# Kernel optimization log

Measured on AMD Instinct MI355X. Metric: run time of the kernel, lower is better.

The kernel has to match this reference:

```python
import jax, jax.numpy as jnp
import numpy as np
from jax import lax

NUM_CHANNELS = 32
PROT_SECTION = 4
PROT_SIZE = NUM_CHANNELS * PROT_SECTION  # 128
BATCH = 128
SEQ_LEN = 8194


def setup_inputs() -> dict:
    key = jax.random.key(0)
    ks = jax.random.split(key, 6)
    input_seq = jax.random.randint(ks[0], (BATCH, SEQ_LEN), 0, 26)
    emb = jax.random.normal(ks[1], (26, 5), dtype=jnp.float32)
    conv_w = jax.random.normal(ks[2], (NUM_CHANNELS, 5, 3), dtype=jnp.float32) * 0.1
    conv_b = jnp.zeros((NUM_CHANNELS,), dtype=jnp.float32)
    W_a = jax.random.normal(ks[3], (PROT_SIZE, PROT_SIZE), dtype=jnp.float32) / np.sqrt(PROT_SIZE)
    v_a = jax.random.normal(ks[4], (PROT_SIZE,), dtype=jnp.float32)
    return {"input_seq": input_seq, "emb": emb, "conv_w": conv_w,
            "conv_b": conv_b, "W_a": W_a, "v_a": v_a}


def reference(input_seq, emb, conv_w, conv_b, W_a, v_a):
    # Embedding lookup: [B, L, 5] -> [B, 5, L]
    x = emb[input_seq].transpose(0, 2, 1)
    # Conv1d(5 -> C, k=3, valid) + bias + ReLU  (dropout is identity in eval)
    y = lax.conv_general_dilated(x, conv_w, window_strides=(1,), padding='VALID',
                                 dimension_numbers=('NCH', 'OIH', 'NCH'))
    y = jax.nn.relu(y + conv_b[None, :, None])  # [B, C, L-2]
    B, C, PL = y.shape
    S = PROT_SECTION
    new_L = PL // S
    rem = PL % S
    head = rem // 2
    tail = PL - (rem - head)
    y = y[:, :, head:tail].reshape(B, C * S, new_L)  # [B, D, N], D = C*S
    # Batched self-attention pooling (original loops over batch in Python)
    # energies[b, n] = v_a @ tanh(W_a @ H_b)
    e = jnp.einsum('d,bdn->bn', v_a, jnp.tanh(jnp.einsum('de,ben->bdn', W_a, y)))
    w = jax.nn.softmax(e, axis=-1)  # stable softmax; same math as unstable F.softmax
    ctx = jnp.einsum('bn,bdn->bd', w, y)  # [B, D]
    return ctx
```

## Files before the change

### kernel.cpp

```cpp
#include <hip/hip_runtime.h>

#define LSEQ 8194
#define NPOS 2048

typedef _Float16 f16x8 __attribute__((ext_vector_type(8)));
typedef _Float16 f16x2 __attribute__((ext_vector_type(2)));
typedef __attribute__((ext_vector_type(4))) float f32x4;

static __device__ __forceinline__ float tanh_fast(float x){
    float p = __expf(2.0f * x);
    float r = __builtin_amdgcn_rcpf(1.0f + p);
    return 1.0f - 2.0f * r;
}
static __device__ __forceinline__ unsigned h3relu(unsigned a, unsigned b, unsigned c){
    union { f16x2 h; unsigned u; } x, y, z, r;
    x.u = a; y.u = b; z.u = c;
    f16x2 s = x.h + y.h + z.h;
    f16x2 zero = { (_Float16)0.0f, (_Float16)0.0f };
    r.h = __builtin_elementwise_max(s, zero);
    return r.u;
}
static __device__ __forceinline__ unsigned hpack(float a, float b){
    union { f16x2 h; unsigned u; } pk;
    pk.h = (f16x2){ (_Float16)a, (_Float16)b };
    return pk.u;
}

__global__ __launch_bounds__(256) void k_tbl(
        const float* __restrict__ emb, const float* __restrict__ cw,
        const float* __restrict__ cb, const float* __restrict__ Wa,
        unsigned* __restrict__ tblp, unsigned* __restrict__ wah)
{
    int gid = blockIdx.x*256 + threadIdx.x;
    if (gid < 1248){
        int k = gid / 416;
        int rem = gid - k*416;
        int l = rem >> 4;
        int cp = rem & 15;
        int c0 = cp*2;
        float v0 = 0.f, v1 = 0.f;
        #pragma unroll
        for (int i = 0; i < 5; i++){
            float e = emb[l*5 + i];
            v0 += cw[(c0*5 + i)*3 + k] * e;
            v1 += cw[((c0+1)*5 + i)*3 + k] * e;
        }
        if (k == 2){ v0 += cb[c0]; v1 += cb[c0+1]; }
        tblp[k*520 + l*20 + (cp & 3)*4 + (cp >> 2)] = hpack(v0, v1);
    }
    for (int i = gid; i < 8192; i += 1280)
        wah[i] = hpack(Wa[2*i], Wa[2*i + 1]);
}

__global__ __launch_bounds__(256, 4) void ka_conv_gemm(
        const int* __restrict__ seq, const unsigned* __restrict__ tblp,
        const unsigned* __restrict__ wah, const float* __restrict__ va,
        float* __restrict__ ws_e)
{
    __shared__ __align__(16) unsigned tblH[1560];
    __shared__ unsigned short seqw16[4][132];
    __shared__ uint4 bshare[16*64];
    __shared__ float epar[4][64];

    int tid = threadIdx.x;
    int b   = blockIdx.y;
    int n0  = blockIdx.x * 128;

    for (int i = tid; i < 390; i += 256)
        ((uint4*)tblH)[i] = ((const uint4*)tblp)[i];
    const int* sb = seq + (size_t)b * LSEQ;
    for (int i = tid; i < 4*130; i += 256){
        int s = i / 130, off = i - s*130;
        seqw16[s][off] = (unsigned short)(sb[s*2048 + n0 + off] * 80);
    }

    int w = tid >> 6, lane = tid & 63;
    int m = lane & 15, q = lane >> 4;

    uint4 wfu[2][4];
    #pragma unroll
    for (int dtL = 0; dtL < 2; dtL++)
        #pragma unroll
        for (int ki = 0; ki < 4; ki++)
            wfu[dtL][ki] = *(const uint4*)((const char*)wah +
                ((2*w+dtL)*16 + m)*256 + ki*64 + q*16);
    float varg[2][4];
    #pragma unroll
    for (int dtL = 0; dtL < 2; dtL++)
        #pragma unroll
        for (int r = 0; r < 4; r++)
            varg[dtL][r] = va[(2*w+dtL)*16 + q*4 + r];
    __syncthreads();

    const char* tb0 = (const char*)tblH + q*16;
    const char* tb1 = tb0 + 2080;
    const char* tb2 = tb1 + 2080;

    for (int sub = 0; sub < 2; sub++){
        int row = sub*64 + w*16 + m;
        unsigned o0[4], o1[4], o2[4];
        #pragma unroll
        for (int s = 0; s < 4; s++){
            o0[s] = seqw16[s][row];
            o1[s] = seqw16[s][row+1];
            o2[s] = seqw16[s][row+2];
        }
        unsigned V[4][4];
        #pragma unroll
        for (int s = 0; s < 4; s++){
            uint4 t0 = *(const uint4*)(tb0 + o0[s]);
            uint4 t1 = *(const uint4*)(tb1 + o1[s]);
            uint4 t2 = *(const uint4*)(tb2 + o2[s]);
            V[s][0] = h3relu(t0.x, t1.x, t2.x);
            V[s][1] = h3relu(t0.y, t1.y, t2.y);
            V[s][2] = h3relu(t0.z, t1.z, t2.z);
            V[s][3] = h3relu(t0.w, t1.w, t2.w);
        }
        #pragma unroll
        for (int ki = 0; ki < 4; ki++){
            uint4 o;
            o.x = __builtin_amdgcn_perm(V[1][ki], V[0][ki], 0x05040100u);
            o.y = __builtin_amdgcn_perm(V[3][ki], V[2][ki], 0x05040100u);
            o.z = __builtin_amdgcn_perm(V[1][ki], V[0][ki], 0x07060302u);
            o.w = __builtin_amdgcn_perm(V[3][ki], V[2][ki], 0x07060302u);
            bshare[(w*4 + ki)*64 + lane] = o;
        }
        __syncthreads();

        f32x4 acc[2][4];
        #pragma unroll
        for (int dtL = 0; dtL < 2; dtL++)
            #pragma unroll
            for (int rg = 0; rg < 4; rg++) acc[dtL][rg] = (f32x4){0.f,0.f,0.f,0.f};
        #pragma unroll
        for (int rg = 0; rg < 4; rg++){
            #pragma unroll
            for (int ki = 0; ki < 4; ki++){
                union { uint4 u; f16x8 f; } bu, a0, a1;
                bu.u = bshare[(rg*4 + ki)*64 + lane];
                a0.u = wfu[0][ki];
                a1.u = wfu[1][ki];
                acc[0][rg] = __builtin_amdgcn_mfma_f32_16x16x32_f16(a0.f, bu.f, acc[0][rg], 0, 0, 0);
                acc[1][rg] = __builtin_amdgcn_mfma_f32_16x16x32_f16(a1.f, bu.f, acc[1][rg], 0, 0, 0);
            }
        }
        #pragma unroll
        for (int rg = 0; rg < 4; rg++){
            float ep = 0.f;
            #pragma unroll
            for (int dtL = 0; dtL < 2; dtL++){
                ep += varg[dtL][0] * tanh_fast(acc[dtL][rg][0]);
                ep += varg[dtL][1] * tanh_fast(acc[dtL][rg][1]);
                ep += varg[dtL][2] * tanh_fast(acc[dtL][rg][2]);
                ep += varg[dtL][3] * tanh_fast(acc[dtL][rg][3]);
            }
            ep += __shfl_xor(ep, 16);
            ep += __shfl_xor(ep, 32);
            if (lane < 16) epar[w][rg*16 + lane] = ep;
        }
        __syncthreads();
        if (tid < 64){
            float e4 = epar[0][tid] + epar[1][tid] + epar[2][tid] + epar[3][tid];
            ws_e[b*NPOS + n0 + sub*64 + tid] = e4;
        }
    }
}

__global__ __launch_bounds__(256, 4) void kb1_pool(
        const int* __restrict__ seq, const unsigned* __restrict__ tblp,
        const float* __restrict__ ws_e, float* __restrict__ part)
{
    __shared__ __align__(16) unsigned tblH[1560];
    __shared__ unsigned short seqw16[4][260];
    __shared__ float wlds[256];
    __shared__ float red[4], red2[4];
    __shared__ float red3[4][4][32];

    int tid = threadIdx.x;
    int b = blockIdx.y;
    int x = blockIdx.x;
    int n0 = x * 256;

    for (int i = tid; i < 390; i += 256)
        ((uint4*)tblH)[i] = ((const uint4*)tblp)[i];
    const int* sb = seq + (size_t)b * LSEQ;
    for (int i = tid; i < 4*258; i += 256){
        int s = i / 258, off = i - s*258;
        seqw16[s][off] = (unsigned short)(sb[s*2048 + n0 + off] * 80);
    }

    const float* e = ws_e + b*NPOS;
    float ev[8];
    #pragma unroll
    for (int r = 0; r < 8; r++) ev[r] = e[tid + r*256];
    int wave = tid >> 6, lane = tid & 63;
    float mx = -1e30f;
    #pragma unroll
    for (int r = 0; r < 8; r++) mx = fmaxf(mx, ev[r]);
    #pragma unroll
    for (int off = 32; off >= 1; off >>= 1) mx = fmaxf(mx, __shfl_xor(mx, off));
    if (lane == 0) red[wave] = mx;
    __syncthreads();
    mx = fmaxf(fmaxf(red[0], red[1]), fmaxf(red[2], red[3]));
    float sum = 0.f;
    #pragma unroll
    for (int r = 0; r < 8; r++) sum += __expf(ev[r] - mx);
    #pragma unroll
    for (int off = 32; off >= 1; off >>= 1) sum += __shfl_xor(sum, off);
    if (lane == 0) red2[wave] = sum;
    __syncthreads();
    float rs = 1.0f / (red2[0] + red2[1] + red2[2] + red2[3]);
    wlds[tid] = __expf(e[n0 + tid] - mx) * rs;
    __syncthreads();

    int qq = tid & 3, nn = tid >> 2;
    const char* t0 = (const char*)tblH + qq*16;
    const char* t1 = t0 + 2080;
    const char* t2 = t1 + 2080;
    float acc[32];
    #pragma unroll
    for (int j = 0; j < 32; j++) acc[j] = 0.f;
    for (int it = 0; it < 4; it++){
        int n = it*64 + nn;
        float wgt = wlds[n];
        unsigned o0[4], o1[4], o2[4];
        #pragma unroll
        for (int s = 0; s < 4; s++){
            o0[s] = seqw16[s][n];
            o1[s] = seqw16[s][n+1];
            o2[s] = seqw16[s][n+2];
        }
        #pragma unroll
        for (int s = 0; s < 4; s++){
            uint4 a = *(const uint4*)(t0 + o0[s]);
            uint4 bb = *(const uint4*)(t1 + o1[s]);
            uint4 c = *(const uint4*)(t2 + o2[s]);
            union { f16x2 h; unsigned u; } u0, u1, u2, u3;
            u0.u = h3relu(a.x, bb.x, c.x);
            u1.u = h3relu(a.y, bb.y, c.y);
            u2.u = h3relu(a.z, bb.z, c.z);
            u3.u = h3relu(a.w, bb.w, c.w);
            acc[0*8 + 0*4 + s] += wgt * (float)u0.h[0];
            acc[0*8 + 1*4 + s] += wgt * (float)u0.h[1];
            acc[1*8 + 0*4 + s] += wgt * (float)u1.h[0];
            acc[1*8 + 1*4 + s] += wgt * (float)u1.h[1];
            acc[2*8 + 0*4 + s] += wgt * (float)u2.h[0];
            acc[2*8 + 1*4 + s] += wgt * (float)u2.h[1];
            acc[3*8 + 0*4 + s] += wgt * (float)u3.h[0];
            acc[3*8 + 1*4 + s] += wgt * (float)u3.h[1];
        }
    }
    #pragma unroll
    for (int j = 0; j < 32; j++){
        acc[j] += __shfl_xor(acc[j], 4);
        acc[j] += __shfl_xor(acc[j], 8);
        acc[j] += __shfl_xor(acc[j], 16);
        acc[j] += __shfl_xor(acc[j], 32);
    }
    if (lane < 4){
        #pragma unroll
        for (int j = 0; j < 32; j++) red3[wave][lane][j] = acc[j];
    }
    __syncthreads();
    if (tid < 128){
        int ki = tid >> 5, q2 = (tid >> 3) & 3, par = (tid >> 2) & 1, s = tid & 3;
        int a = ki*8 + par*4 + s;
        part[((size_t)b*8 + x)*128 + tid] =
            red3[0][q2][a] + red3[1][q2][a] + red3[2][q2][a] + red3[3][q2][a];
    }
}

__global__ __launch_bounds__(128) void kb2_finish(const float* __restrict__ part,
        float* __restrict__ out)
{
    int b = blockIdx.x, d = threadIdx.x;
    const float* p = part + (size_t)b*8*128 + d;
    float s = 0.f;
    #pragma unroll
    for (int x = 0; x < 8; x++) s += p[x*128];
    out[b*128 + d] = s;
}

extern "C" void kernel_launch(void* const* d_in, const int* in_sizes, int n_in,
                              void* d_out, int out_size, void* d_ws, size_t ws_size,
                              hipStream_t stream)
{
    const int*   seq = (const int*)d_in[0];
    const float* emb = (const float*)d_in[1];
    const float* cw  = (const float*)d_in[2];
    const float* cb  = (const float*)d_in[3];
    const float* Wa  = (const float*)d_in[4];
    const float* va  = (const float*)d_in[5];
    float* out = (float*)d_out;

    char* wsb = (char*)d_ws;
    float*    ws_e = (float*)wsb;
    float*    part = (float*)(wsb + (1<<20));
    unsigned* tblp = (unsigned*)(wsb + (2<<20));
    unsigned* wah  = (unsigned*)(wsb + (2<<20) + 16384);

    k_tbl       <<<5,            256, 0, stream>>>(emb, cw, cb, Wa, tblp, wah);
    ka_conv_gemm<<<dim3(16,128), 256, 0, stream>>>(seq, tblp, wah, va, ws_e);
    kb1_pool    <<<dim3(8,128),  256, 0, stream>>>(seq, tblp, ws_e, part);
    kb2_finish  <<<128,          128, 0, stream>>>(part, out);
}
```

Before: 106.1 us.

## Fuse energy GEMM and pooling into one kernel with split softmax merge

Merges the conv+GEMM energy kernel and the pooling kernel into a single kernel. Each block computes the energies for its own 256 positions and a local max and sum, then pools with unnormalised local weights. The finish kernel rescales the partials using the per-block statistics, in the style of flash-attention. This removes one launch, the round trip of the energies through global memory, and the repeated table and sequence staging, but it halves the grid (1024 blocks instead of 2048) and makes each block do more serial work.

```diff
diff --git a/kernel.cpp b/kernel.cpp
--- a/kernel.cpp
+++ b/kernel.cpp
@@ -52,25 +52,30 @@
         wah[i] = hpack(Wa[2*i], Wa[2*i + 1]);
 }
 
-__global__ __launch_bounds__(256, 4) void ka_conv_gemm(
+__global__ __launch_bounds__(256, 4) void k_fused(
         const int* __restrict__ seq, const unsigned* __restrict__ tblp,
         const unsigned* __restrict__ wah, const float* __restrict__ va,
-        float* __restrict__ ws_e)
+        float* __restrict__ part, float* __restrict__ stats)
 {
     __shared__ __align__(16) unsigned tblH[1560];
-    __shared__ unsigned short seqw16[4][132];
+    __shared__ unsigned short seqw16[4][260];
     __shared__ uint4 bshare[16*64];
     __shared__ float epar[4][64];
+    __shared__ float elds[256];
+    __shared__ float wlds[256];
+    __shared__ float red[4], red2[4];
+    __shared__ float red3[4][4][32];
 
     int tid = threadIdx.x;
     int b   = blockIdx.y;
-    int n0  = blockIdx.x * 128;
+    int x   = blockIdx.x;
+    int n0  = x * 256;
 
     for (int i = tid; i < 390; i += 256)
         ((uint4*)tblH)[i] = ((const uint4*)tblp)[i];
     const int* sb = seq + (size_t)b * LSEQ;
-    for (int i = tid; i < 4*130; i += 256){
-        int s = i / 130, off = i - s*130;
+    for (int i = tid; i < 4*258; i += 256){
+        int s = i / 258, off = i - s*258;
         seqw16[s][off] = (unsigned short)(sb[s*2048 + n0 + off] * 80);
     }
 
@@ -96,7 +101,7 @@
     const char* tb1 = tb0 + 2080;
     const char* tb2 = tb1 + 2080;
 
-    for (int sub = 0; sub < 2; sub++){
+    for (int sub = 0; sub < 4; sub++){
         int row = sub*64 + w*16 + m;
         unsigned o0[4], o1[4], o2[4];
         #pragma unroll
@@ -159,59 +164,26 @@
             if (lane < 16) epar[w][rg*16 + lane] = ep;
         }
         __syncthreads();
-        if (tid < 64){
-            float e4 = epar[0][tid] + epar[1][tid] + epar[2][tid] + epar[3][tid];
-            ws_e[b*NPOS + n0 + sub*64 + tid] = e4;
-        }
-    }
-}
-
-__global__ __launch_bounds__(256, 4) void kb1_pool(
-        const int* __restrict__ seq, const unsigned* __restrict__ tblp,
-        const float* __restrict__ ws_e, float* __restrict__ part)
-{
-    __shared__ __align__(16) unsigned tblH[1560];
-    __shared__ unsigned short seqw16[4][260];
-    __shared__ float wlds[256];
-    __shared__ float red[4], red2[4];
-    __shared__ float red3[4][4][32];
-
-    int tid = threadIdx.x;
-    int b = blockIdx.y;
-    int x = blockIdx.x;
-    int n0 = x * 256;
-
-    for (int i = tid; i < 390; i += 256)
-        ((uint4*)tblH)[i] = ((const uint4*)tblp)[i];
-    const int* sb = seq + (size_t)b * LSEQ;
-    for (int i = tid; i < 4*258; i += 256){
-        int s = i / 258, off = i - s*258;
-        seqw16[s][off] = (unsigned short)(sb[s*2048 + n0 + off] * 80);
-    }
-
-    const float* e = ws_e + b*NPOS;
-    float ev[8];
-    #pragma unroll
-    for (int r = 0; r < 8; r++) ev[r] = e[tid + r*256];
-    int wave = tid >> 6, lane = tid & 63;
-    float mx = -1e30f;
-    #pragma unroll
-    for (int r = 0; r < 8; r++) mx = fmaxf(mx, ev[r]);
+        if (tid < 64)
+            elds[sub*64 + tid] = epar[0][tid] + epar[1][tid] + epar[2][tid] + epar[3][tid];
+    }
+    __syncthreads();
+
+    float ev = elds[tid];
+    float mx = ev;
     #pragma unroll
     for (int off = 32; off >= 1; off >>= 1) mx = fmaxf(mx, __shfl_xor(mx, off));
-    if (lane == 0) red[wave] = mx;
+    if (lane == 0) red[w] = mx;
     __syncthreads();
     mx = fmaxf(fmaxf(red[0], red[1]), fmaxf(red[2], red[3]));
-    float sum = 0.f;
-    #pragma unroll
-    for (int r = 0; r < 8; r++) sum += __expf(ev[r] - mx);
+    float wgt_own = __expf(ev - mx);
+    float sum = wgt_own;
     #pragma unroll
     for (int off = 32; off >= 1; off >>= 1) sum += __shfl_xor(sum, off);
-    if (lane == 0) red2[wave] = sum;
-    __syncthreads();
-    float rs = 1.0f / (red2[0] + red2[1] + red2[2] + red2[3]);
-    wlds[tid] = __expf(e[n0 + tid] - mx) * rs;
-    __syncthreads();
+    if (lane == 0) red2[w] = sum;
+    wlds[tid] = wgt_own;
+    __syncthreads();
+    float s_x = red2[0] + red2[1] + red2[2] + red2[3];
 
     int qq = tid & 3, nn = tid >> 2;
     const char* t0 = (const char*)tblH + qq*16;
@@ -259,7 +231,7 @@
     }
     if (lane < 4){
         #pragma unroll
-        for (int j = 0; j < 32; j++) red3[wave][lane][j] = acc[j];
+        for (int j = 0; j < 32; j++) red3[w][lane][j] = acc[j];
     }
     __syncthreads();
     if (tid < 128){
@@ -268,17 +240,32 @@
         part[((size_t)b*8 + x)*128 + tid] =
             red3[0][q2][a] + red3[1][q2][a] + red3[2][q2][a] + red3[3][q2][a];
     }
+    if (tid == 0){
+        stats[((size_t)b*8 + x)*2    ] = mx;
+        stats[((size_t)b*8 + x)*2 + 1] = s_x;
+    }
 }
 
 __global__ __launch_bounds__(128) void kb2_finish(const float* __restrict__ part,
-        float* __restrict__ out)
+        const float* __restrict__ stats, float* __restrict__ out)
 {
     int b = blockIdx.x, d = threadIdx.x;
+    const float* st = stats + (size_t)b*16;
+    float M = -1e30f;
+    #pragma unroll
+    for (int x = 0; x < 8; x++) M = fmaxf(M, st[x*2]);
+    float f[8], S = 0.f;
+    #pragma unroll
+    for (int x = 0; x < 8; x++){
+        f[x] = __expf(st[x*2] - M);
+        S += st[x*2+1] * f[x];
+    }
+    float inv = 1.0f / S;
     const float* p = part + (size_t)b*8*128 + d;
     float s = 0.f;
     #pragma unroll
-    for (int x = 0; x < 8; x++) s += p[x*128];
-    out[b*128 + d] = s;
+    for (int x = 0; x < 8; x++) s += p[x*128] * f[x];
+    out[b*128 + d] = s * inv;
 }
 
 extern "C" void kernel_launch(void* const* d_in, const int* in_sizes, int n_in,
@@ -294,13 +281,12 @@
     float* out = (float*)d_out;
 
     char* wsb = (char*)d_ws;
-    float*    ws_e = (float*)wsb;
-    float*    part = (float*)(wsb + (1<<20));
-    unsigned* tblp = (unsigned*)(wsb + (2<<20));
-    unsigned* wah  = (unsigned*)(wsb + (2<<20) + 16384);
-
-    k_tbl       <<<5,            256, 0, stream>>>(emb, cw, cb, Wa, tblp, wah);
-    ka_conv_gemm<<<dim3(16,128), 256, 0, stream>>>(seq, tblp, wah, va, ws_e);
-    kb1_pool    <<<dim3(8,128),  256, 0, stream>>>(seq, tblp, ws_e, part);
-    kb2_finish  <<<128,          128, 0, stream>>>(part, out);
-}
+    float*    part  = (float*)wsb;
+    float*    stats = (float*)(wsb + (1<<20));
+    unsigned* tblp  = (unsigned*)(wsb + (2<<20));
+    unsigned* wah   = (unsigned*)(wsb + (2<<20) + 16384);
+
+    k_tbl     <<<5,           256, 0, stream>>>(emb, cw, cb, Wa, tblp, wah);
+    k_fused   <<<dim3(8,128), 256, 0, stream>>>(seq, tblp, wah, va, part, stats);
+    kb2_finish<<<128,         128, 0, stream>>>(part, stats, out);
+}
```

Result: faster. 98.34 us (-7.3%).
